# Performance work log

Hardware: AMD Instinct MI355X
Metric: run time of the kernel (lower is better)

Reference implementation:

```python
import jax, jax.numpy as jnp
import numpy as np

B, L, DM, H, PD = 2, 1024, 512, 8, 64
D = DM // H  # head_dim = 64
NEG = -10000.0


def setup_inputs() -> dict:
    key = jax.random.key(0)
    ks = jax.random.split(key, 12)
    s = 1.0 / np.sqrt(DM)
    sp = 1.0 / np.sqrt(PD)
    return {
        "x": jax.random.normal(ks[0], (B, L, DM), dtype=jnp.float32),
        "z": jax.random.normal(ks[1], (B, L, L, PD), dtype=jnp.float32),
        "residue_mask": jnp.ones((B, L), dtype=bool),
        "Wq": jax.random.normal(ks[2], (DM, DM), dtype=jnp.float32) * s,
        "bq": jnp.zeros((DM,), dtype=jnp.float32),
        "Wk": jax.random.normal(ks[3], (DM, DM), dtype=jnp.float32) * s,
        "bk": jnp.zeros((DM,), dtype=jnp.float32),
        "Wv": jax.random.normal(ks[4], (DM, DM), dtype=jnp.float32) * s,
        "bv": jnp.zeros((DM,), dtype=jnp.float32),
        "Wo": jax.random.normal(ks[5], (DM, DM), dtype=jnp.float32) * s,
        "bo": jnp.zeros((DM,), dtype=jnp.float32),
        "Wpb": jax.random.normal(ks[6], (PD, H), dtype=jnp.float32) * sp,
    }


def reference(x, z, residue_mask, Wq, bq, Wk, bk, Wv, bv, Wo, bo, Wpb):
    b, l, c = x.shape
    scale = 1.0 / np.sqrt(D)
    # projections -> (B, H, L, D)
    q = (x @ Wq + bq).reshape(b, l, H, D).transpose(0, 2, 1, 3)
    k = (x @ Wk + bk).reshape(b, l, H, D).transpose(0, 2, 1, 3)
    v = (x @ Wv + bv).reshape(b, l, H, D).transpose(0, 2, 1, 3)
    # pair bias: (B, L, L, PD) @ (PD, H) -> (B, H, L, L)
    bias = jnp.einsum('bijp,ph->bhij', z, Wpb)
    logits = jnp.einsum('bhid,bhjd->bhij', q, k) * scale + bias
    key_ok = residue_mask[:, None, None, :]
    query_ok = residue_mask[:, None, :, None]
    logits = jnp.where(key_ok, logits, NEG)
    logits = jnp.where(query_ok, logits, NEG)
    attn = jax.nn.softmax(logits, axis=-1)
    out = jnp.einsum('bhij,bhjd->bhid', attn, v)
    out = out.transpose(0, 2, 1, 3).reshape(b, l, c)
    return out @ Wo + bo
```

## Files before the change

### kernel.cpp

```cpp
#include <hip/hip_runtime.h>

typedef __bf16 bf16;
typedef __attribute__((ext_vector_type(4))) __bf16 bf16x4;
typedef __attribute__((ext_vector_type(8))) __bf16 bf16x8;
typedef __attribute__((ext_vector_type(4))) float f32x4;
typedef __attribute__((ext_vector_type(4))) _Float16 f16x4;
typedef __attribute__((ext_vector_type(2))) _Float16 f16x2;

#define B_   2
#define L_   1024
#define DM_  512
#define H_   8
#define D_   64
#define PD_  64
#define NEG_VAL -10000.0f

#define XB_N   (2048*512)
#define WT_N   (1536*512)
#define WTO_N  (512*512)
#define WTPB_N (16*64)

static __device__ __forceinline__ f32x4 mfma_bf16(bf16x8 a, bf16x8 b, f32x4 c) {
  return __builtin_amdgcn_mfma_f32_16x16x32_bf16(a, b, c, 0, 0, 0);
}

__global__ __launch_bounds__(256) void prep_kernel(
    const float* __restrict__ x, const float* __restrict__ Wq, const float* __restrict__ Wk,
    const float* __restrict__ Wv, const float* __restrict__ Wo, const float* __restrict__ Wpb,
    bf16* __restrict__ xb, bf16* __restrict__ Wt, bf16* __restrict__ Wto, bf16* __restrict__ Wtpb) {
  const int total = XB_N + WT_N + WTO_N + WTPB_N;
  for (int idx = blockIdx.x * 256 + threadIdx.x; idx < total; idx += gridDim.x * 256) {
    if (idx < XB_N) {
      xb[idx] = (bf16)x[idx];
    } else if (idx < XB_N + WT_N) {
      int t = idx - XB_N;
      int n = t >> 9, kk = t & 511;
      int sel = n >> 9, nn = n & 511;
      const float* W = sel == 0 ? Wq : (sel == 1 ? Wk : Wv);
      Wt[t] = (bf16)W[kk * 512 + nn];
    } else if (idx < XB_N + WT_N + WTO_N) {
      int t = idx - XB_N - WT_N;
      int n = t >> 9, kk = t & 511;
      Wto[t] = (bf16)Wo[kk * 512 + n];
    } else {
      int t = idx - XB_N - WT_N - WTO_N;
      int n = t >> 6, kk = t & 63;
      Wtpb[t] = (n < 8) ? (bf16)Wpb[kk * 8 + n] : (bf16)0.0f;
    }
  }
}

__global__ __launch_bounds__(256) void qkv_gemm(
    const bf16* __restrict__ xb, const bf16* __restrict__ Wt,
    const float* __restrict__ bq, const float* __restrict__ bk, const float* __restrict__ bv,
    bf16* __restrict__ qb, bf16* __restrict__ kb, bf16* __restrict__ vT) {
  int wid = blockIdx.x * 4 + (threadIdx.x >> 6);
  int lane = threadIdx.x & 63;
  int mt = wid / 48, nt = wid - mt * 48;
  int row0 = mt * 32, col0 = nt * 32;
  int lr = lane & 15, lg = lane >> 4;
  const bf16* a0p = xb + (row0 + lr) * 512 + lg * 8;
  const bf16* a1p = a0p + 16 * 512;
  const bf16* b0p = Wt + (col0 + lr) * 512 + lg * 8;
  const bf16* b1p = b0p + 16 * 512;
  f32x4 acc00 = {0.f,0.f,0.f,0.f}, acc01 = acc00, acc10 = acc00, acc11 = acc00;
#pragma unroll
  for (int kk = 0; kk < 512; kk += 32) {
    bf16x8 a0 = *reinterpret_cast<const bf16x8*>(a0p + kk);
    bf16x8 a1 = *reinterpret_cast<const bf16x8*>(a1p + kk);
    bf16x8 b0 = *reinterpret_cast<const bf16x8*>(b0p + kk);
    bf16x8 b1 = *reinterpret_cast<const bf16x8*>(b1p + kk);
    acc00 = mfma_bf16(a0, b0, acc00);
    acc01 = mfma_bf16(a0, b1, acc01);
    acc10 = mfma_bf16(a1, b0, acc10);
    acc11 = mfma_bf16(a1, b1, acc11);
  }
#pragma unroll
  for (int ni = 0; ni < 2; ++ni) {
    int col = col0 + ni * 16 + lr;
    int wsel = col >> 9;
    int ncol = col & 511;
    int h = ncol >> 6, d = ncol & 63;
    const float* bias = wsel == 0 ? bq : (wsel == 1 ? bk : bv);
    float bval = bias[ncol];
#pragma unroll
    for (int mi = 0; mi < 2; ++mi) {
      f32x4 acc = (mi == 0) ? (ni == 0 ? acc00 : acc01) : (ni == 0 ? acc10 : acc11);
      int m0 = row0 + mi * 16 + lg * 4;
      int bidx = m0 >> 10, l0 = m0 & 1023;
      if (wsel == 2) {
        bf16x4 pv;
#pragma unroll
        for (int r = 0; r < 4; ++r) pv[r] = (bf16)(acc[r] + bval);
        *reinterpret_cast<bf16x4*>(vT + ((long)(bidx * H_ + h) * D_ + d) * L_ + l0) = pv;
      } else if (wsel == 0) {
#pragma unroll
        for (int r = 0; r < 4; ++r)
          qb[((long)(bidx * H_ + h) * L_ + l0 + r) * D_ + d] = (bf16)((acc[r] + bval) * 0.125f);
      } else {
#pragma unroll
        for (int r = 0; r < 4; ++r)
          kb[((long)(bidx * H_ + h) * L_ + l0 + r) * D_ + d] = (bf16)(acc[r] + bval);
      }
    }
  }
}

__global__ __launch_bounds__(256) void bias_gemm(
    const float* __restrict__ z, const bf16* __restrict__ Wtpb, const int* __restrict__ mask,
    _Float16* __restrict__ biasbuf) {
  __shared__ float zt_raw[64 * 64];
  __shared__ _Float16 bt[8][72];
  int tid = threadIdx.x;
  int w = tid >> 6, lane = tid & 63;
  int lr = lane & 15, lg = lane >> 4;
  char* zb = (char*)zt_raw;
  const char* zsrc = (const char*)(z + (long)blockIdx.x * 4096);
#pragma unroll
  for (int q = 0; q < 4; ++q) {
    int lb = q * 4096 + tid * 16;
    int row = lb >> 8, col = lb & 255;
    f32x4 v = *reinterpret_cast<const f32x4*>(zsrc + lb);
    *reinterpret_cast<f32x4*>(zb + row * 256 + (col ^ ((row & 7) << 5))) = v;
  }
  bf16x8 b0 = *reinterpret_cast<const bf16x8*>(Wtpb + lr * 64 + lg * 8);
  bf16x8 b1 = *reinterpret_cast<const bf16x8*>(Wtpb + lr * 64 + 32 + lg * 8);
  __syncthreads();
  int row = w * 16 + lr;
  int sw = (row & 7) << 5;
  const char* zr = zb + row * 256;
  f32x4 z0 = *reinterpret_cast<const f32x4*>(zr + ((lg * 32) ^ sw));
  f32x4 z1 = *reinterpret_cast<const f32x4*>(zr + (((lg * 32) ^ sw) + 16));
  f32x4 z2 = *reinterpret_cast<const f32x4*>(zr + ((128 + lg * 32) ^ sw));
  f32x4 z3 = *reinterpret_cast<const f32x4*>(zr + (((128 + lg * 32) ^ sw) + 16));
  bf16x8 a0, a1;
#pragma unroll
  for (int e = 0; e < 4; ++e) { a0[e] = (bf16)z0[e]; a0[e + 4] = (bf16)z1[e]; }
#pragma unroll
  for (int e = 0; e < 4; ++e) { a1[e] = (bf16)z2[e]; a1[e + 4] = (bf16)z3[e]; }
  f32x4 acc = {0.f, 0.f, 0.f, 0.f};
  acc = mfma_bf16(a0, b0, acc);
  acc = mfma_bf16(a1, b1, acc);
  __syncthreads();
  if (lr < 8) {
    f16x4 hv;
#pragma unroll
    for (int r = 0; r < 4; ++r) hv[r] = (_Float16)acc[r];
    *reinterpret_cast<f16x4*>(&bt[lr][w * 16 + lg * 4]) = hv;
  }
  __syncthreads();
  {
    int h = tid >> 5, part = tid & 31;
    long pb = (long)blockIdx.x * 64;
    int b = (int)(pb >> 20), i = ((int)(pb >> 10)) & 1023, j0 = (int)pb & 1023;
    int j = j0 + part * 2;
    f16x2 v = *reinterpret_cast<const f16x2*>(&bt[h][part * 2]);
    if (mask[b * L_ + j] == 0)     v[0] = (_Float16)NEG_VAL;
    if (mask[b * L_ + j + 1] == 0) v[1] = (_Float16)NEG_VAL;
    _Float16* dst = biasbuf + ((((long)b * H_ + h) * L_ + i) << 10) + j;
    *reinterpret_cast<f16x2*>(dst) = v;
  }
}

__global__ __launch_bounds__(256) void attn_part(
    const bf16* __restrict__ qb, const bf16* __restrict__ kb, const bf16* __restrict__ vT,
    const _Float16* __restrict__ biasb, const int* __restrict__ mask,
    float* __restrict__ part_o, float* __restrict__ part_m, float* __restrict__ part_l) {
  __shared__ bf16 p_lds[4][16 * 64];
  int bid = blockIdx.x;
  int jc = bid & 1, it = (bid >> 1) & 63, h = (bid >> 7) & 7, b = bid >> 10;
  int i0 = it * 16;
  int tid = threadIdx.x, w = tid >> 6, lane = tid & 63, lr = lane & 15, lg = lane >> 4;

  const bf16* qrow = qb + ((long)(b * H_ + h) * L_ + i0 + lr) * D_ + lg * 8;
  bf16x8 qa0 = *reinterpret_cast<const bf16x8*>(qrow);
  bf16x8 qa1 = *reinterpret_cast<const bf16x8*>(qrow + 32);
  const bf16* kbase = kb + (long)(b * H_ + h) * L_ * D_;
  const bf16* vbase = vT + (long)(b * H_ + h) * D_ * L_;
  const _Float16* bias_base = biasb + ((long)(b * H_ + h) * L_ + i0) * L_;
  bool qok = mask[b * L_ + i0 + lr] != 0;

  float m = -3.0e38f, l = 0.f;
  f32x4 o0 = {0.f,0.f,0.f,0.f}, o1 = o0, o2 = o0, o3 = o0;
  char* pbuf = (char*)&p_lds[w][0];
  int swz = (lr & 7) << 4;
  int jbase = jc * 512 + w * 128;

  for (int jt = 0; jt < 2; ++jt) {
    int j0 = jbase + jt * 64;
    f32x4 s0, s1, s2, s3;
#pragma unroll
    for (int tile = 0; tile < 4; ++tile) {
      f16x4 bv = *reinterpret_cast<const f16x4*>(bias_base + (long)lr * L_ + j0 + tile * 16 + lg * 4);
      f32x4 acc;
#pragma unroll
      for (int r = 0; r < 4; ++r) acc[r] = (float)bv[r];
      const bf16* kr = kbase + (long)(j0 + tile * 16 + lr) * D_ + lg * 8;
      acc = mfma_bf16(*reinterpret_cast<const bf16x8*>(kr), qa0, acc);
      acc = mfma_bf16(*reinterpret_cast<const bf16x8*>(kr + 32), qa1, acc);
      if (tile == 0) s0 = acc; else if (tile == 1) s1 = acc; else if (tile == 2) s2 = acc; else s3 = acc;
    }
    if (!qok) {
#pragma unroll
      for (int r = 0; r < 4; ++r) { s0[r] = NEG_VAL; s1[r] = NEG_VAL; s2[r] = NEG_VAL; s3[r] = NEG_VAL; }
    }
    float mt = s0[0];
#pragma unroll
    for (int r = 0; r < 4; ++r) mt = fmaxf(fmaxf(fmaxf(mt, s0[r]), fmaxf(s1[r], s2[r])), s3[r]);
    mt = fmaxf(mt, __shfl_xor(mt, 16));
    mt = fmaxf(mt, __shfl_xor(mt, 32));
    float mnew = fmaxf(m, mt);
    float alpha = __expf(m - mnew);
    m = mnew;
    f32x4 p0, p1, p2, p3;
    float ps = 0.f;
#pragma unroll
    for (int r = 0; r < 4; ++r) {
      p0[r] = __expf(s0[r] - mnew); p1[r] = __expf(s1[r] - mnew);
      p2[r] = __expf(s2[r] - mnew); p3[r] = __expf(s3[r] - mnew);
      ps += p0[r] + p1[r] + p2[r] + p3[r];
    }
    ps += __shfl_xor(ps, 16);
    ps += __shfl_xor(ps, 32);
    l = l * alpha + ps;
#pragma unroll
    for (int r = 0; r < 4; ++r) { o0[r] *= alpha; o1[r] *= alpha; o2[r] *= alpha; o3[r] *= alpha; }
#pragma unroll
    for (int tile = 0; tile < 4; ++tile) {
      f32x4 pv = (tile == 0) ? p0 : (tile == 1) ? p1 : (tile == 2) ? p2 : p3;
      bf16x4 pb_;
#pragma unroll
      for (int r = 0; r < 4; ++r) pb_[r] = (bf16)pv[r];
      *reinterpret_cast<bf16x4*>(pbuf + ((lr * 128 + tile * 32 + lg * 8) ^ swz)) = pb_;
    }
    bf16x8 pa0 = *reinterpret_cast<const bf16x8*>(pbuf + ((lr * 128 + lg * 16) ^ swz));
    bf16x8 pa1 = *reinterpret_cast<const bf16x8*>(pbuf + ((lr * 128 + 64 + lg * 16) ^ swz));
#pragma unroll
    for (int dtile = 0; dtile < 4; ++dtile) {
      const bf16* vr = vbase + (long)(dtile * 16 + lr) * L_ + j0 + lg * 8;
      f32x4 acc = (dtile == 0) ? o0 : (dtile == 1) ? o1 : (dtile == 2) ? o2 : o3;
      acc = mfma_bf16(*reinterpret_cast<const bf16x8*>(vr), pa0, acc);
      acc = mfma_bf16(*reinterpret_cast<const bf16x8*>(vr + 32), pa1, acc);
      if (dtile == 0) o0 = acc; else if (dtile == 1) o1 = acc; else if (dtile == 2) o2 = acc; else o3 = acc;
    }
  }
  int wid = bid * 4 + w;
  float* po = part_o + (long)wid * 1024;
#pragma unroll
  for (int dtile = 0; dtile < 4; ++dtile) {
    f32x4 ov = (dtile == 0) ? o0 : (dtile == 1) ? o1 : (dtile == 2) ? o2 : o3;
    *reinterpret_cast<f32x4*>(po + lr * 64 + dtile * 16 + lg * 4) = ov;
  }
  if (lg == 0) { part_m[wid * 16 + lr] = m; part_l[wid * 16 + lr] = l; }
}

__global__ __launch_bounds__(256) void merge8(
    const float* __restrict__ part_o, const float* __restrict__ part_m,
    const float* __restrict__ part_l, bf16* __restrict__ attn_out) {
  int t = blockIdx.x * 256 + threadIdx.x;
  int d0 = (t & 15) * 4;
  int row = t >> 4;
  int b = row >> 13, h = (row >> 10) & 7, i = row & 1023;
  int it = i >> 4, il = i & 15;
  int bid0 = ((b * H_ + h) * 64 + it) * 2;
  float mv[8];
  float M = -3.0e38f;
#pragma unroll
  for (int p = 0; p < 8; ++p) {
    int wid = (bid0 + (p >> 2)) * 4 + (p & 3);
    mv[p] = part_m[wid * 16 + il];
    M = fmaxf(M, mv[p]);
  }
  float lt = 0.f;
  float oa[4] = {0.f, 0.f, 0.f, 0.f};
#pragma unroll
  for (int p = 0; p < 8; ++p) {
    int wid = (bid0 + (p >> 2)) * 4 + (p & 3);
    float c = __expf(mv[p] - M);
    lt += c * part_l[wid * 16 + il];
    f32x4 ov = *reinterpret_cast<const f32x4*>(part_o + ((long)wid * 16 + il) * 64 + d0);
#pragma unroll
    for (int e = 0; e < 4; ++e) oa[e] += c * ov[e];
  }
  float inv = 1.0f / lt;
  bf16x4 r_;
#pragma unroll
  for (int e = 0; e < 4; ++e) r_[e] = (bf16)(oa[e] * inv);
  *reinterpret_cast<bf16x4*>(attn_out + ((long)(b * L_ + i)) * DM_ + h * D_ + d0) = r_;
}

__global__ __launch_bounds__(256) void out_gemm(
    const bf16* __restrict__ ab, const bf16* __restrict__ Wto,
    const float* __restrict__ bo, float* __restrict__ out) {
  int wid = blockIdx.x * 4 + (threadIdx.x >> 6);
  int lane = threadIdx.x & 63;
  int mt = wid >> 4, nt = wid & 15;
  int row0 = mt * 32, col0 = nt * 32;
  int lr = lane & 15, lg = lane >> 4;
  const bf16* a0p = ab + (row0 + lr) * 512 + lg * 8;
  const bf16* a1p = a0p + 16 * 512;
  const bf16* b0p = Wto + (col0 + lr) * 512 + lg * 8;
  const bf16* b1p = b0p + 16 * 512;
  f32x4 acc00 = {0.f,0.f,0.f,0.f}, acc01 = acc00, acc10 = acc00, acc11 = acc00;
#pragma unroll
  for (int kk = 0; kk < 512; kk += 32) {
    bf16x8 a0 = *reinterpret_cast<const bf16x8*>(a0p + kk);
    bf16x8 a1 = *reinterpret_cast<const bf16x8*>(a1p + kk);
    bf16x8 b0 = *reinterpret_cast<const bf16x8*>(b0p + kk);
    bf16x8 b1 = *reinterpret_cast<const bf16x8*>(b1p + kk);
    acc00 = mfma_bf16(a0, b0, acc00);
    acc01 = mfma_bf16(a0, b1, acc01);
    acc10 = mfma_bf16(a1, b0, acc10);
    acc11 = mfma_bf16(a1, b1, acc11);
  }
#pragma unroll
  for (int ni = 0; ni < 2; ++ni) {
    int col = col0 + ni * 16 + lr;
    float bval = bo[col];
#pragma unroll
    for (int mi = 0; mi < 2; ++mi) {
      f32x4 acc = (mi == 0) ? (ni == 0 ? acc00 : acc01) : (ni == 0 ? acc10 : acc11);
      int m0 = row0 + mi * 16 + lg * 4;
#pragma unroll
      for (int r = 0; r < 4; ++r) out[(long)(m0 + r) * 512 + col] = acc[r] + bval;
    }
  }
}

extern "C" void kernel_launch(void* const* d_in, const int* in_sizes, int n_in,
                              void* d_out, int out_size, void* d_ws, size_t ws_size,
                              hipStream_t stream) {
  const float* x    = (const float*)d_in[0];
  const float* z    = (const float*)d_in[1];
  const int*   mask = (const int*)d_in[2];
  const float* Wq   = (const float*)d_in[3];
  const float* bq   = (const float*)d_in[4];
  const float* Wk   = (const float*)d_in[5];
  const float* bk   = (const float*)d_in[6];
  const float* Wv   = (const float*)d_in[7];
  const float* bv   = (const float*)d_in[8];
  const float* Wo   = (const float*)d_in[9];
  const float* bo   = (const float*)d_in[10];
  const float* Wpb  = (const float*)d_in[11];

  char* ws = (char*)d_ws;
  bf16* xb        = (bf16*)(ws + 0);
  bf16* Wt        = (bf16*)(ws + 2097152);
  bf16* Wto       = (bf16*)(ws + 3670016);
  bf16* Wtpb      = (bf16*)(ws + 4194304);
  bf16* qbuf      = (bf16*)(ws + 4196352);
  bf16* kbuf      = (bf16*)(ws + 6293504);
  bf16* vTbuf     = (bf16*)(ws + 8390656);
  bf16* attn_out  = (bf16*)(ws + 10487808);
  _Float16* biasb = (_Float16*)(ws + 12584960);
  float* part_o   = (float*)(ws + 46139392);
  float* part_m   = (float*)(ws + 79693824);
  float* part_l   = (float*)(ws + 80218112);

  prep_kernel<<<2048, 256, 0, stream>>>(x, Wq, Wk, Wv, Wo, Wpb, xb, Wt, Wto, Wtpb);
  qkv_gemm<<<768, 256, 0, stream>>>(xb, Wt, bq, bk, bv, qbuf, kbuf, vTbuf);
  bias_gemm<<<32768, 256, 0, stream>>>(z, Wtpb, mask, biasb);
  attn_part<<<2048, 256, 0, stream>>>(qbuf, kbuf, vTbuf, biasb, mask, part_o, part_m, part_l);
  merge8<<<1024, 256, 0, stream>>>(part_o, part_m, part_l, attn_out);
  out_gemm<<<256, 256, 0, stream>>>(attn_out, Wto, bo, (float*)d_out);
}
```

Baseline: 202.2 us.

## Fuse pair-bias projection into attention kernel and merge 16 key-chunk partials

Removes the separate bias_gemm pass and its f16 bias buffer round-trip. Each attention block now reads a 16x64 tile of z, projects it to all 8 heads into LDS, and then each wave handles two heads over one 64-key chunk. Partial outputs are stored as f16 and combined by a 16-way merge kernel. This saves the bias write/read traffic and one launch, at the cost of more partial-output traffic, a wider merge, and f16 precision on the partials.

```diff
diff --git a/kernel.cpp b/kernel.cpp
--- a/kernel.cpp
+++ b/kernel.cpp
@@ -106,125 +106,105 @@
   }
 }
 
-__global__ __launch_bounds__(256) void bias_gemm(
-    const float* __restrict__ z, const bf16* __restrict__ Wtpb, const int* __restrict__ mask,
-    _Float16* __restrict__ biasbuf) {
-  __shared__ float zt_raw[64 * 64];
-  __shared__ _Float16 bt[8][72];
-  int tid = threadIdx.x;
-  int w = tid >> 6, lane = tid & 63;
-  int lr = lane & 15, lg = lane >> 4;
-  char* zb = (char*)zt_raw;
-  const char* zsrc = (const char*)(z + (long)blockIdx.x * 4096);
-#pragma unroll
-  for (int q = 0; q < 4; ++q) {
-    int lb = q * 4096 + tid * 16;
-    int row = lb >> 8, col = lb & 255;
-    f32x4 v = *reinterpret_cast<const f32x4*>(zsrc + lb);
-    *reinterpret_cast<f32x4*>(zb + row * 256 + (col ^ ((row & 7) << 5))) = v;
-  }
-  bf16x8 b0 = *reinterpret_cast<const bf16x8*>(Wtpb + lr * 64 + lg * 8);
-  bf16x8 b1 = *reinterpret_cast<const bf16x8*>(Wtpb + lr * 64 + 32 + lg * 8);
-  __syncthreads();
-  int row = w * 16 + lr;
-  int sw = (row & 7) << 5;
-  const char* zr = zb + row * 256;
-  f32x4 z0 = *reinterpret_cast<const f32x4*>(zr + ((lg * 32) ^ sw));
-  f32x4 z1 = *reinterpret_cast<const f32x4*>(zr + (((lg * 32) ^ sw) + 16));
-  f32x4 z2 = *reinterpret_cast<const f32x4*>(zr + ((128 + lg * 32) ^ sw));
-  f32x4 z3 = *reinterpret_cast<const f32x4*>(zr + (((128 + lg * 32) ^ sw) + 16));
-  bf16x8 a0, a1;
-#pragma unroll
-  for (int e = 0; e < 4; ++e) { a0[e] = (bf16)z0[e]; a0[e + 4] = (bf16)z1[e]; }
-#pragma unroll
-  for (int e = 0; e < 4; ++e) { a1[e] = (bf16)z2[e]; a1[e + 4] = (bf16)z3[e]; }
-  f32x4 acc = {0.f, 0.f, 0.f, 0.f};
-  acc = mfma_bf16(a0, b0, acc);
-  acc = mfma_bf16(a1, b1, acc);
-  __syncthreads();
-  if (lr < 8) {
-    f16x4 hv;
-#pragma unroll
-    for (int r = 0; r < 4; ++r) hv[r] = (_Float16)acc[r];
-    *reinterpret_cast<f16x4*>(&bt[lr][w * 16 + lg * 4]) = hv;
-  }
-  __syncthreads();
-  {
-    int h = tid >> 5, part = tid & 31;
-    long pb = (long)blockIdx.x * 64;
-    int b = (int)(pb >> 20), i = ((int)(pb >> 10)) & 1023, j0 = (int)pb & 1023;
-    int j = j0 + part * 2;
-    f16x2 v = *reinterpret_cast<const f16x2*>(&bt[h][part * 2]);
-    if (mask[b * L_ + j] == 0)     v[0] = (_Float16)NEG_VAL;
-    if (mask[b * L_ + j + 1] == 0) v[1] = (_Float16)NEG_VAL;
-    _Float16* dst = biasbuf + ((((long)b * H_ + h) * L_ + i) << 10) + j;
-    *reinterpret_cast<f16x2*>(dst) = v;
-  }
-}
-
-__global__ __launch_bounds__(256) void attn_part(
-    const bf16* __restrict__ qb, const bf16* __restrict__ kb, const bf16* __restrict__ vT,
-    const _Float16* __restrict__ biasb, const int* __restrict__ mask,
-    float* __restrict__ part_o, float* __restrict__ part_m, float* __restrict__ part_l) {
+__global__ __launch_bounds__(256) void fused_attn(
+    const float* __restrict__ z, const bf16* __restrict__ qb, const bf16* __restrict__ kb,
+    const bf16* __restrict__ vT, const bf16* __restrict__ Wtpb, const int* __restrict__ mask,
+    _Float16* __restrict__ part_o, float* __restrict__ part_m, float* __restrict__ part_l) {
+  __shared__ _Float16 bias_lds[8 * 16 * 64];
   __shared__ bf16 p_lds[4][16 * 64];
   int bid = blockIdx.x;
-  int jc = bid & 1, it = (bid >> 1) & 63, h = (bid >> 7) & 7, b = bid >> 10;
-  int i0 = it * 16;
+  int jc = bid & 15, it = (bid >> 4) & 63, b = bid >> 10;
+  int i0 = it * 16, j0 = jc * 64;
   int tid = threadIdx.x, w = tid >> 6, lane = tid & 63, lr = lane & 15, lg = lane >> 4;
 
-  const bf16* qrow = qb + ((long)(b * H_ + h) * L_ + i0 + lr) * D_ + lg * 8;
-  bf16x8 qa0 = *reinterpret_cast<const bf16x8*>(qrow);
-  bf16x8 qa1 = *reinterpret_cast<const bf16x8*>(qrow + 32);
-  const bf16* kbase = kb + (long)(b * H_ + h) * L_ * D_;
-  const bf16* vbase = vT + (long)(b * H_ + h) * D_ * L_;
-  const _Float16* bias_base = biasb + ((long)(b * H_ + h) * L_ + i0) * L_;
+  bf16x8 wb0 = *reinterpret_cast<const bf16x8*>(Wtpb + lr * 64 + lg * 8);
+  bf16x8 wb1 = *reinterpret_cast<const bf16x8*>(Wtpb + lr * 64 + 32 + lg * 8);
+
+  {
+    char* bl = (char*)bias_lds;
+#pragma unroll
+    for (int ii = 0; ii < 4; ++ii) {
+      int i = w * 4 + ii;
+      const float* zb_ = z + ((long)(b * L_ + i0 + i) * L_ + j0) * 64;
+#pragma unroll
+      for (int js = 0; js < 4; ++js) {
+        const float* zr = zb_ + (js * 16 + lr) * 64 + lg * 8;
+        f32x4 f0 = *reinterpret_cast<const f32x4*>(zr);
+        f32x4 f1 = *reinterpret_cast<const f32x4*>(zr + 4);
+        f32x4 f2 = *reinterpret_cast<const f32x4*>(zr + 32);
+        f32x4 f3 = *reinterpret_cast<const f32x4*>(zr + 36);
+        bf16x8 a0, a1;
+#pragma unroll
+        for (int e = 0; e < 4; ++e) {
+          a0[e] = (bf16)f0[e]; a0[e + 4] = (bf16)f1[e];
+          a1[e] = (bf16)f2[e]; a1[e + 4] = (bf16)f3[e];
+        }
+        f32x4 c = {0.f, 0.f, 0.f, 0.f};
+        c = mfma_bf16(a0, wb0, c);
+        c = mfma_bf16(a1, wb1, c);
+        if (lr < 8) {
+          f16x4 hv;
+#pragma unroll
+          for (int r = 0; r < 4; ++r) hv[r] = (_Float16)c[r];
+          int X = (js * 32 + lg * 8) ^ ((i & 7) << 4) ^ ((lr & 3) << 5);
+          *reinterpret_cast<f16x4*>(bl + lr * 2048 + i * 128 + X) = hv;
+        }
+      }
+    }
+  }
+  __syncthreads();
+
   bool qok = mask[b * L_ + i0 + lr] != 0;
-
-  float m = -3.0e38f, l = 0.f;
-  f32x4 o0 = {0.f,0.f,0.f,0.f}, o1 = o0, o2 = o0, o3 = o0;
   char* pbuf = (char*)&p_lds[w][0];
   int swz = (lr & 7) << 4;
-  int jbase = jc * 512 + w * 128;
-
-  for (int jt = 0; jt < 2; ++jt) {
-    int j0 = jbase + jt * 64;
+  const char* bl = (const char*)bias_lds;
+
+#pragma unroll
+  for (int hh = 0; hh < 2; ++hh) {
+    int h = w * 2 + hh;
+    const bf16* qrow = qb + ((long)(b * H_ + h) * L_ + i0 + lr) * D_ + lg * 8;
+    bf16x8 qa0 = *reinterpret_cast<const bf16x8*>(qrow);
+    bf16x8 qa1 = *reinterpret_cast<const bf16x8*>(qrow + 32);
+    const bf16* kbase = kb + (long)(b * H_ + h) * L_ * D_;
+    const bf16* vbase = vT + (long)(b * H_ + h) * D_ * L_;
+
     f32x4 s0, s1, s2, s3;
 #pragma unroll
     for (int tile = 0; tile < 4; ++tile) {
-      f16x4 bv = *reinterpret_cast<const f16x4*>(bias_base + (long)lr * L_ + j0 + tile * 16 + lg * 4);
+      int X = (tile * 32 + lg * 8) ^ ((lr & 7) << 4) ^ ((h & 3) << 5);
+      f16x4 bv = *reinterpret_cast<const f16x4*>(bl + h * 2048 + lr * 128 + X);
       f32x4 acc;
 #pragma unroll
       for (int r = 0; r < 4; ++r) acc[r] = (float)bv[r];
       const bf16* kr = kbase + (long)(j0 + tile * 16 + lr) * D_ + lg * 8;
       acc = mfma_bf16(*reinterpret_cast<const bf16x8*>(kr), qa0, acc);
       acc = mfma_bf16(*reinterpret_cast<const bf16x8*>(kr + 32), qa1, acc);
+      int4 mk = *reinterpret_cast<const int4*>(mask + b * L_ + j0 + tile * 16 + lg * 4);
+      if (mk.x == 0) acc[0] = NEG_VAL;
+      if (mk.y == 0) acc[1] = NEG_VAL;
+      if (mk.z == 0) acc[2] = NEG_VAL;
+      if (mk.w == 0) acc[3] = NEG_VAL;
       if (tile == 0) s0 = acc; else if (tile == 1) s1 = acc; else if (tile == 2) s2 = acc; else s3 = acc;
     }
     if (!qok) {
 #pragma unroll
       for (int r = 0; r < 4; ++r) { s0[r] = NEG_VAL; s1[r] = NEG_VAL; s2[r] = NEG_VAL; s3[r] = NEG_VAL; }
     }
-    float mt = s0[0];
-#pragma unroll
-    for (int r = 0; r < 4; ++r) mt = fmaxf(fmaxf(fmaxf(mt, s0[r]), fmaxf(s1[r], s2[r])), s3[r]);
-    mt = fmaxf(mt, __shfl_xor(mt, 16));
-    mt = fmaxf(mt, __shfl_xor(mt, 32));
-    float mnew = fmaxf(m, mt);
-    float alpha = __expf(m - mnew);
-    m = mnew;
+    float m = s0[0];
+#pragma unroll
+    for (int r = 0; r < 4; ++r) m = fmaxf(fmaxf(fmaxf(m, s0[r]), fmaxf(s1[r], s2[r])), s3[r]);
+    m = fmaxf(m, __shfl_xor(m, 16));
+    m = fmaxf(m, __shfl_xor(m, 32));
     f32x4 p0, p1, p2, p3;
     float ps = 0.f;
 #pragma unroll
     for (int r = 0; r < 4; ++r) {
-      p0[r] = __expf(s0[r] - mnew); p1[r] = __expf(s1[r] - mnew);
-      p2[r] = __expf(s2[r] - mnew); p3[r] = __expf(s3[r] - mnew);
+      p0[r] = __expf(s0[r] - m); p1[r] = __expf(s1[r] - m);
+      p2[r] = __expf(s2[r] - m); p3[r] = __expf(s3[r] - m);
       ps += p0[r] + p1[r] + p2[r] + p3[r];
     }
     ps += __shfl_xor(ps, 16);
     ps += __shfl_xor(ps, 32);
-    l = l * alpha + ps;
-#pragma unroll
-    for (int r = 0; r < 4; ++r) { o0[r] *= alpha; o1[r] *= alpha; o2[r] *= alpha; o3[r] *= alpha; }
 #pragma unroll
     for (int tile = 0; tile < 4; ++tile) {
       f32x4 pv = (tile == 0) ? p0 : (tile == 1) ? p1 : (tile == 2) ? p2 : p3;
@@ -235,52 +215,49 @@
     }
     bf16x8 pa0 = *reinterpret_cast<const bf16x8*>(pbuf + ((lr * 128 + lg * 16) ^ swz));
     bf16x8 pa1 = *reinterpret_cast<const bf16x8*>(pbuf + ((lr * 128 + 64 + lg * 16) ^ swz));
+    long obase = ((long)bid * H_ + h) * 16;
 #pragma unroll
     for (int dtile = 0; dtile < 4; ++dtile) {
       const bf16* vr = vbase + (long)(dtile * 16 + lr) * L_ + j0 + lg * 8;
-      f32x4 acc = (dtile == 0) ? o0 : (dtile == 1) ? o1 : (dtile == 2) ? o2 : o3;
+      f32x4 acc = {0.f, 0.f, 0.f, 0.f};
       acc = mfma_bf16(*reinterpret_cast<const bf16x8*>(vr), pa0, acc);
       acc = mfma_bf16(*reinterpret_cast<const bf16x8*>(vr + 32), pa1, acc);
-      if (dtile == 0) o0 = acc; else if (dtile == 1) o1 = acc; else if (dtile == 2) o2 = acc; else o3 = acc;
-    }
-  }
-  int wid = bid * 4 + w;
-  float* po = part_o + (long)wid * 1024;
-#pragma unroll
-  for (int dtile = 0; dtile < 4; ++dtile) {
-    f32x4 ov = (dtile == 0) ? o0 : (dtile == 1) ? o1 : (dtile == 2) ? o2 : o3;
-    *reinterpret_cast<f32x4*>(po + lr * 64 + dtile * 16 + lg * 4) = ov;
-  }
-  if (lg == 0) { part_m[wid * 16 + lr] = m; part_l[wid * 16 + lr] = l; }
-}
-
-__global__ __launch_bounds__(256) void merge8(
-    const float* __restrict__ part_o, const float* __restrict__ part_m,
+      f16x4 ov;
+#pragma unroll
+      for (int r = 0; r < 4; ++r) ov[r] = (_Float16)acc[r];
+      *reinterpret_cast<f16x4*>(part_o + (obase + lr) * 64 + dtile * 16 + lg * 4) = ov;
+    }
+    if (lg == 0) { part_m[obase + lr] = m; part_l[obase + lr] = ps; }
+  }
+}
+
+__global__ __launch_bounds__(256) void merge16(
+    const _Float16* __restrict__ part_o, const float* __restrict__ part_m,
     const float* __restrict__ part_l, bf16* __restrict__ attn_out) {
   int t = blockIdx.x * 256 + threadIdx.x;
   int d0 = (t & 15) * 4;
   int row = t >> 4;
   int b = row >> 13, h = (row >> 10) & 7, i = row & 1023;
   int it = i >> 4, il = i & 15;
-  int bid0 = ((b * H_ + h) * 64 + it) * 2;
-  float mv[8];
+  int bid0 = (b << 10) + (it << 4);
+  float mv[16];
   float M = -3.0e38f;
 #pragma unroll
-  for (int p = 0; p < 8; ++p) {
-    int wid = (bid0 + (p >> 2)) * 4 + (p & 3);
-    mv[p] = part_m[wid * 16 + il];
+  for (int p = 0; p < 16; ++p) {
+    long base = ((long)(bid0 + p) * H_ + h) * 16 + il;
+    mv[p] = part_m[base];
     M = fmaxf(M, mv[p]);
   }
   float lt = 0.f;
   float oa[4] = {0.f, 0.f, 0.f, 0.f};
 #pragma unroll
-  for (int p = 0; p < 8; ++p) {
-    int wid = (bid0 + (p >> 2)) * 4 + (p & 3);
+  for (int p = 0; p < 16; ++p) {
+    long base = ((long)(bid0 + p) * H_ + h) * 16 + il;
     float c = __expf(mv[p] - M);
-    lt += c * part_l[wid * 16 + il];
-    f32x4 ov = *reinterpret_cast<const f32x4*>(part_o + ((long)wid * 16 + il) * 64 + d0);
-#pragma unroll
-    for (int e = 0; e < 4; ++e) oa[e] += c * ov[e];
+    lt += c * part_l[base];
+    f16x4 ov = *reinterpret_cast<const f16x4*>(part_o + base * 64 + d0);
+#pragma unroll
+    for (int e = 0; e < 4; ++e) oa[e] += c * (float)ov[e];
   }
   float inv = 1.0f / lt;
   bf16x4 r_;
@@ -352,15 +329,13 @@
   bf16* kbuf      = (bf16*)(ws + 6293504);
   bf16* vTbuf     = (bf16*)(ws + 8390656);
   bf16* attn_out  = (bf16*)(ws + 10487808);
-  _Float16* biasb = (_Float16*)(ws + 12584960);
-  float* part_o   = (float*)(ws + 46139392);
-  float* part_m   = (float*)(ws + 79693824);
-  float* part_l   = (float*)(ws + 80218112);
+  _Float16* part_o = (_Float16*)(ws + 12584960);
+  float* part_m   = (float*)(ws + 46139392);
+  float* part_l   = (float*)(ws + 47187968);
 
   prep_kernel<<<2048, 256, 0, stream>>>(x, Wq, Wk, Wv, Wo, Wpb, xb, Wt, Wto, Wtpb);
   qkv_gemm<<<768, 256, 0, stream>>>(xb, Wt, bq, bk, bv, qbuf, kbuf, vTbuf);
-  bias_gemm<<<32768, 256, 0, stream>>>(z, Wtpb, mask, biasb);
-  attn_part<<<2048, 256, 0, stream>>>(qbuf, kbuf, vTbuf, biasb, mask, part_o, part_m, part_l);
-  merge8<<<1024, 256, 0, stream>>>(part_o, part_m, part_l, attn_out);
+  fused_attn<<<2048, 256, 0, stream>>>(z, qbuf, kbuf, vTbuf, Wtpb, mask, part_o, part_m, part_l);
+  merge16<<<1024, 256, 0, stream>>>(part_o, part_m, part_l, attn_out);
   out_gemm<<<256, 256, 0, stream>>>(attn_out, Wto, bo, (float*)d_out);
 }
```

New measurement: 188.5 us. 1.07x faster.

## Fuse split-KV merge into attention kernel and tile weight transpose via LDS

Applied to the files above, without the earlier changes.

The attention kernel now handles a full 16-row query tile per block, with four waves each covering 256 keys. The partial results are merged in shared memory, which removes the merge8 kernel and its global round-trip of partial outputs. The prep kernel now transposes weights through a 32x33 LDS tile with vectorised loads and stores instead of strided scalar reads. The output GEMM is relaunched as one wave per block. Halving the attention grid lowers parallelism and adds LDS use, but the dominant bias_gemm is unchanged.

```diff
diff --git a/kernel.cpp b/kernel.cpp
--- a/kernel.cpp
+++ b/kernel.cpp
@@ -15,9 +15,6 @@
 #define PD_  64
 #define NEG_VAL -10000.0f
 
-#define XB_N   (2048*512)
-#define WT_N   (1536*512)
-#define WTO_N  (512*512)
 #define WTPB_N (16*64)
 
 static __device__ __forceinline__ f32x4 mfma_bf16(bf16x8 a, bf16x8 b, f32x4 c) {
@@ -28,22 +25,45 @@
     const float* __restrict__ x, const float* __restrict__ Wq, const float* __restrict__ Wk,
     const float* __restrict__ Wv, const float* __restrict__ Wo, const float* __restrict__ Wpb,
     bf16* __restrict__ xb, bf16* __restrict__ Wt, bf16* __restrict__ Wto, bf16* __restrict__ Wtpb) {
-  const int total = XB_N + WT_N + WTO_N + WTPB_N;
-  for (int idx = blockIdx.x * 256 + threadIdx.x; idx < total; idx += gridDim.x * 256) {
-    if (idx < XB_N) {
-      xb[idx] = (bf16)x[idx];
-    } else if (idx < XB_N + WT_N) {
-      int t = idx - XB_N;
-      int n = t >> 9, kk = t & 511;
-      int sel = n >> 9, nn = n & 511;
-      const float* W = sel == 0 ? Wq : (sel == 1 ? Wk : Wv);
-      Wt[t] = (bf16)W[kk * 512 + nn];
-    } else if (idx < XB_N + WT_N + WTO_N) {
-      int t = idx - XB_N - WT_N;
-      int n = t >> 9, kk = t & 511;
-      Wto[t] = (bf16)Wo[kk * 512 + n];
+  __shared__ float td[32][33];
+  int bid = blockIdx.x, tid = threadIdx.x;
+  if (bid < 1024) {
+    int r = tid >> 3, c4 = (tid & 7) * 4;
+    const float* src;
+    bf16* dstbase;
+    int n0, k0, srcol;
+    if (bid < 768) {
+      int nt2 = bid >> 4, kt = bid & 15;
+      n0 = nt2 * 32; k0 = kt * 32;
+      int sel = n0 >> 9;
+      src = sel == 0 ? Wq : (sel == 1 ? Wk : Wv);
+      srcol = n0 & 511;
+      dstbase = Wt + (long)n0 * 512;
     } else {
-      int t = idx - XB_N - WT_N - WTO_N;
+      int t2 = bid - 768;
+      int nt2 = t2 >> 4, kt = t2 & 15;
+      n0 = nt2 * 32; k0 = kt * 32;
+      src = Wo; srcol = n0;
+      dstbase = Wto + (long)n0 * 512;
+    }
+    f32x4 v = *reinterpret_cast<const f32x4*>(src + (long)(k0 + r) * 512 + srcol + c4);
+#pragma unroll
+    for (int e = 0; e < 4; ++e) td[r][c4 + e] = v[e];
+    __syncthreads();
+    int nl = tid >> 3, k4 = (tid & 7) * 4;
+    bf16x4 o;
+#pragma unroll
+    for (int e = 0; e < 4; ++e) o[e] = (bf16)td[k4 + e][nl];
+    *reinterpret_cast<bf16x4*>(dstbase + (long)nl * 512 + k0 + k4) = o;
+  } else if (bid < 2048) {
+    int base = (bid - 1024) * 1024 + tid * 4;
+    f32x4 v = *reinterpret_cast<const f32x4*>(x + base);
+    bf16x4 o;
+#pragma unroll
+    for (int e = 0; e < 4; ++e) o[e] = (bf16)v[e];
+    *reinterpret_cast<bf16x4*>(xb + base) = o;
+  } else {
+    for (int t = tid; t < WTPB_N; t += 256) {
       int n = t >> 6, kk = t & 63;
       Wtpb[t] = (n < 8) ? (bf16)Wpb[kk * 8 + n] : (bf16)0.0f;
     }
@@ -162,13 +182,15 @@
   }
 }
 
-__global__ __launch_bounds__(256) void attn_part(
+__global__ __launch_bounds__(256) void attn_kernel(
     const bf16* __restrict__ qb, const bf16* __restrict__ kb, const bf16* __restrict__ vT,
-    const _Float16* __restrict__ biasb, const int* __restrict__ mask,
-    float* __restrict__ part_o, float* __restrict__ part_m, float* __restrict__ part_l) {
+    const _Float16* __restrict__ biasb, const int* __restrict__ mask, bf16* __restrict__ attn_out) {
   __shared__ bf16 p_lds[4][16 * 64];
+  __shared__ float o_lds[4][16][64];
+  __shared__ float m_lds[4][16];
+  __shared__ float l_lds[4][16];
   int bid = blockIdx.x;
-  int jc = bid & 1, it = (bid >> 1) & 63, h = (bid >> 7) & 7, b = bid >> 10;
+  int b = bid >> 9, h = (bid >> 6) & 7, it = bid & 63;
   int i0 = it * 16;
   int tid = threadIdx.x, w = tid >> 6, lane = tid & 63, lr = lane & 15, lg = lane >> 4;
 
@@ -184,10 +206,9 @@
   f32x4 o0 = {0.f,0.f,0.f,0.f}, o1 = o0, o2 = o0, o3 = o0;
   char* pbuf = (char*)&p_lds[w][0];
   int swz = (lr & 7) << 4;
-  int jbase = jc * 512 + w * 128;
-
-  for (int jt = 0; jt < 2; ++jt) {
-    int j0 = jbase + jt * 64;
+
+  for (int jt = 0; jt < 4; ++jt) {
+    int j0 = w * 256 + jt * 64;
     f32x4 s0, s1, s2, s3;
 #pragma unroll
     for (int tile = 0; tile < 4; ++tile) {
@@ -244,56 +265,38 @@
       if (dtile == 0) o0 = acc; else if (dtile == 1) o1 = acc; else if (dtile == 2) o2 = acc; else o3 = acc;
     }
   }
-  int wid = bid * 4 + w;
-  float* po = part_o + (long)wid * 1024;
 #pragma unroll
   for (int dtile = 0; dtile < 4; ++dtile) {
     f32x4 ov = (dtile == 0) ? o0 : (dtile == 1) ? o1 : (dtile == 2) ? o2 : o3;
-    *reinterpret_cast<f32x4*>(po + lr * 64 + dtile * 16 + lg * 4) = ov;
-  }
-  if (lg == 0) { part_m[wid * 16 + lr] = m; part_l[wid * 16 + lr] = l; }
-}
-
-__global__ __launch_bounds__(256) void merge8(
-    const float* __restrict__ part_o, const float* __restrict__ part_m,
-    const float* __restrict__ part_l, bf16* __restrict__ attn_out) {
-  int t = blockIdx.x * 256 + threadIdx.x;
-  int d0 = (t & 15) * 4;
-  int row = t >> 4;
-  int b = row >> 13, h = (row >> 10) & 7, i = row & 1023;
-  int it = i >> 4, il = i & 15;
-  int bid0 = ((b * H_ + h) * 64 + it) * 2;
-  float mv[8];
-  float M = -3.0e38f;
-#pragma unroll
-  for (int p = 0; p < 8; ++p) {
-    int wid = (bid0 + (p >> 2)) * 4 + (p & 3);
-    mv[p] = part_m[wid * 16 + il];
-    M = fmaxf(M, mv[p]);
-  }
-  float lt = 0.f;
-  float oa[4] = {0.f, 0.f, 0.f, 0.f};
-#pragma unroll
-  for (int p = 0; p < 8; ++p) {
-    int wid = (bid0 + (p >> 2)) * 4 + (p & 3);
-    float c = __expf(mv[p] - M);
-    lt += c * part_l[wid * 16 + il];
-    f32x4 ov = *reinterpret_cast<const f32x4*>(part_o + ((long)wid * 16 + il) * 64 + d0);
-#pragma unroll
-    for (int e = 0; e < 4; ++e) oa[e] += c * ov[e];
-  }
-  float inv = 1.0f / lt;
-  bf16x4 r_;
-#pragma unroll
-  for (int e = 0; e < 4; ++e) r_[e] = (bf16)(oa[e] * inv);
-  *reinterpret_cast<bf16x4*>(attn_out + ((long)(b * L_ + i)) * DM_ + h * D_ + d0) = r_;
-}
-
-__global__ __launch_bounds__(256) void out_gemm(
+    *reinterpret_cast<f32x4*>(&o_lds[w][lr][dtile * 16 + lg * 4]) = ov;
+  }
+  if (lg == 0) { m_lds[w][lr] = m; l_lds[w][lr] = l; }
+  __syncthreads();
+  {
+    int row = tid >> 4, d0 = (tid & 15) * 4;
+    float M = fmaxf(fmaxf(m_lds[0][row], m_lds[1][row]), fmaxf(m_lds[2][row], m_lds[3][row]));
+    float lt = 0.f;
+    float oacc[4] = {0.f, 0.f, 0.f, 0.f};
+#pragma unroll
+    for (int ww = 0; ww < 4; ++ww) {
+      float c = __expf(m_lds[ww][row] - M);
+      lt += c * l_lds[ww][row];
+#pragma unroll
+      for (int e = 0; e < 4; ++e) oacc[e] += c * o_lds[ww][row][d0 + e];
+    }
+    float inv = 1.0f / lt;
+    bf16x4 ov;
+#pragma unroll
+    for (int e = 0; e < 4; ++e) ov[e] = (bf16)(oacc[e] * inv);
+    *reinterpret_cast<bf16x4*>(attn_out + ((long)(b * L_ + i0 + row)) * DM_ + h * D_ + d0) = ov;
+  }
+}
+
+__global__ __launch_bounds__(64) void out_gemm(
     const bf16* __restrict__ ab, const bf16* __restrict__ Wto,
     const float* __restrict__ bo, float* __restrict__ out) {
-  int wid = blockIdx.x * 4 + (threadIdx.x >> 6);
-  int lane = threadIdx.x & 63;
+  int wid = blockIdx.x;
+  int lane = threadIdx.x;
   int mt = wid >> 4, nt = wid & 15;
   int row0 = mt * 32, col0 = nt * 32;
   int lr = lane & 15, lg = lane >> 4;
@@ -353,14 +356,10 @@
   bf16* vTbuf     = (bf16*)(ws + 8390656);
   bf16* attn_out  = (bf16*)(ws + 10487808);
   _Float16* biasb = (_Float16*)(ws + 12584960);
-  float* part_o   = (float*)(ws + 46139392);
-  float* part_m   = (float*)(ws + 79693824);
-  float* part_l   = (float*)(ws + 80218112);
-
-  prep_kernel<<<2048, 256, 0, stream>>>(x, Wq, Wk, Wv, Wo, Wpb, xb, Wt, Wto, Wtpb);
+
+  prep_kernel<<<2049, 256, 0, stream>>>(x, Wq, Wk, Wv, Wo, Wpb, xb, Wt, Wto, Wtpb);
   qkv_gemm<<<768, 256, 0, stream>>>(xb, Wt, bq, bk, bv, qbuf, kbuf, vTbuf);
   bias_gemm<<<32768, 256, 0, stream>>>(z, Wtpb, mask, biasb);
-  attn_part<<<2048, 256, 0, stream>>>(qbuf, kbuf, vTbuf, biasb, mask, part_o, part_m, part_l);
-  merge8<<<1024, 256, 0, stream>>>(part_o, part_m, part_l, attn_out);
-  out_gemm<<<256, 256, 0, stream>>>(attn_out, Wto, bo, (float*)d_out);
-}
+  attn_kernel<<<1024, 256, 0, stream>>>(qbuf, kbuf, vTbuf, biasb, mask, attn_out);
+  out_gemm<<<1024, 64, 0, stream>>>(attn_out, Wto, bo, (float*)d_out);
+}
```

Result: faster. 192.6 us (-4.7%).
